# Optimization experiments

Hardware: AMD Instinct MI355X
Metric: run time of the kernel (lower is better)

The kernel has to match this reference:

```python
import jax, jax.numpy as jnp
import numpy as np


def setup_inputs() -> dict:
    key = jax.random.key(0)
    ks = jax.random.split(key, 8)
    T, B = 256, 256
    n_m, n_dT, nd, nx = 256, 256, 512, 512
    c = n_m + n_dT + nd  # 1024, RNNCell0 input/hidden size
    s = 0.05  # weight init scale
    return {
        "x": jax.random.normal(ks[0], (B, nx), jnp.float32),
        "M_flow": jax.random.normal(ks[1], (T, B, n_m), jnp.float32),
        "DT": jax.random.normal(ks[2], (T, B, n_dT), jnp.float32),
        "D": jax.random.normal(ks[3], (T, B, nd), jnp.float32),
        # cell0: RNNCell(c, c); cell1: RNNCell(c, nx); bias=False
        "W_ih0": jax.random.normal(ks[4], (c, c), jnp.float32) * s,
        "W_hh0": jax.random.normal(ks[5], (c, c), jnp.float32) * s,
        "W_ih1": jax.random.normal(ks[6], (nx, c), jnp.float32) * s,
        "W_hh1": jax.random.normal(ks[7], (nx, nx), jnp.float32) * s,
    }


def reference(x, M_flow, DT, D, W_ih0, W_hh0, W_ih1, W_hh1):
    # ins per step: cat([m_flow, dT, d], dim=1) -> (T, B, c)
    ins = jnp.concatenate([M_flow, DT, D], axis=2)
    # cell0 receives a freshly zeroed hidden state each step, so its
    # recurrent term W_hh0 @ 0 vanishes; the input->hidden GEMM is
    # therefore time-independent and can be batched over T.
    H = jax.nn.relu(jnp.einsum('tbc,dc->tbd', ins, W_ih0))  # (T, B, c)

    def step(x, h):
        # cell1: x' = relu(W_ih1 @ h + W_hh1 @ x)
        x = jax.nn.relu(h @ W_ih1.T + x @ W_hh1.T)
        return x, x

    _, X = jax.lax.scan(step, x, H)  # X: (T, B, nx)
    Y = X[:, :, -1]                  # y = x[:, -1] per step -> (T, B)
    return X, Y
```

## Files before the change

kernel.cpp:

```cpp
#include <hip/hip_runtime.h>

typedef __attribute__((ext_vector_type(8))) short short8;
typedef __attribute__((ext_vector_type(4))) float f32x4;
typedef __attribute__((ext_vector_type(4))) unsigned int u32x4;

__device__ __forceinline__ unsigned short f2bu(float x) {
  unsigned int u = __float_as_uint(x);
  u += 0x7fffu + ((u >> 16) & 1u);
  return (unsigned short)(u >> 16);
}
__device__ __forceinline__ unsigned int pk2(float a, float b) {
  return (unsigned int)f2bu(a) | ((unsigned int)f2bu(b) << 16);
}
__device__ __forceinline__ void gload_lds16(const void* g, void* l) {
  __builtin_amdgcn_global_load_lds((const __attribute__((address_space(1))) unsigned int*)g,
                                   (__attribute__((address_space(3))) unsigned int*)l, 16, 0, 0);
}
__device__ __forceinline__ void gload_lds16_coh(const void* g, void* l) {
  __builtin_amdgcn_global_load_lds((const __attribute__((address_space(1))) unsigned int*)g,
                                   (__attribute__((address_space(3))) unsigned int*)l, 16, 0, 17);
}
__device__ __forceinline__ void store16_coh(void* p, u32x4 v) {
  asm volatile("global_store_dwordx4 %0, %1, off sc0 sc1" :: "v"(p), "v"(v) : "memory");
}

__global__ void cast_concat_kernel(const float* __restrict__ Mf,
                                   const float* __restrict__ DTf,
                                   const float* __restrict__ Df,
                                   unsigned short* __restrict__ ins) {
  size_t idx = (size_t)blockIdx.x * blockDim.x + threadIdx.x;
  size_t e0 = idx * 8;
  size_t m = e0 >> 10;
  int c = (int)(e0 & 1023);
  const float* src;
  if (c < 256)      src = Mf  + m * 256 + c;
  else if (c < 512) src = DTf + m * 256 + (c - 256);
  else              src = Df  + m * 512 + (c - 512);
  float4 f0 = reinterpret_cast<const float4*>(src)[0];
  float4 f1 = reinterpret_cast<const float4*>(src)[1];
  uint4 o;
  o.x = pk2(f0.x, f0.y); o.y = pk2(f0.z, f0.w);
  o.z = pk2(f1.x, f1.y); o.w = pk2(f1.z, f1.w);
  *reinterpret_cast<uint4*>(ins + e0) = o;
}

__global__ void cast_w_kernel(const float* __restrict__ in, unsigned short* __restrict__ out, int n8) {
  int idx = blockIdx.x * blockDim.x + threadIdx.x;
  if (idx >= n8) return;
  const float* src = in + (size_t)idx * 8;
  float4 f0 = reinterpret_cast<const float4*>(src)[0];
  float4 f1 = reinterpret_cast<const float4*>(src)[1];
  uint4 o;
  o.x = pk2(f0.x, f0.y); o.y = pk2(f0.z, f0.w);
  o.z = pk2(f1.x, f1.y); o.w = pk2(f1.z, f1.w);
  *reinterpret_cast<uint4*>(out + (size_t)idx * 8) = o;
}

template <int RELU, typename TOUT>
__global__ __launch_bounds__(256) void gemm_bt_kernel(const unsigned short* __restrict__ A,
                                                      const unsigned short* __restrict__ Bt,
                                                      TOUT* __restrict__ C,
                                                      int M, int N, int K) {
  __shared__ unsigned short As[128 * 32];
  __shared__ unsigned short Bs[128 * 32];
  const int tid = threadIdx.x;
  const int l = tid & 63, w = tid >> 6;
  const int lr = l & 15, lg = l >> 4;
  const int wm = w >> 1, wn = w & 1;
  const int tiles_n = N >> 7;
  const int tm = blockIdx.x / tiles_n, tn = blockIdx.x % tiles_n;
  const int bm0 = tm << 7, bn0 = tn << 7;

  f32x4 acc[4][4] = {};

  for (int kt = 0; kt < K; kt += 32) {
#pragma unroll
    for (int i = 0; i < 2; ++i) {
      int ch = tid + (i << 8);
      int row = ch >> 2, cc = ch & 3;
      const unsigned short* ga = A + (size_t)(bm0 + row) * K + kt + cc * 8;
      const unsigned short* gb = Bt + (size_t)(bn0 + row) * K + kt + cc * 8;
      unsigned short* la = As + ((size_t)((i << 8) + (w << 6))) * 8;
      unsigned short* lb = Bs + ((size_t)((i << 8) + (w << 6))) * 8;
      gload_lds16(ga, la);
      gload_lds16(gb, lb);
    }
    __syncthreads();
    short8 af[4], bf[4];
#pragma unroll
    for (int mi = 0; mi < 4; ++mi)
      af[mi] = *reinterpret_cast<const short8*>(As + (wm * 64 + mi * 16 + lr) * 32 + lg * 8);
#pragma unroll
    for (int ni = 0; ni < 4; ++ni)
      bf[ni] = *reinterpret_cast<const short8*>(Bs + (wn * 64 + ni * 16 + lr) * 32 + lg * 8);
#pragma unroll
    for (int mi = 0; mi < 4; ++mi)
#pragma unroll
      for (int ni = 0; ni < 4; ++ni)
        acc[mi][ni] = __builtin_amdgcn_mfma_f32_16x16x32_bf16(af[mi], bf[ni], acc[mi][ni], 0, 0, 0);
    __syncthreads();
  }

#pragma unroll
  for (int mi = 0; mi < 4; ++mi)
#pragma unroll
    for (int ni = 0; ni < 4; ++ni)
#pragma unroll
      for (int r = 0; r < 4; ++r) {
        int row = bm0 + wm * 64 + mi * 16 + lg * 4 + r;
        int col = bn0 + wn * 64 + ni * 16 + lr;
        float v = acc[mi][ni][r];
        if (RELU) v = fmaxf(v, 0.f);
        if constexpr (sizeof(TOUT) == 2) {
          reinterpret_cast<unsigned short*>(C)[(size_t)row * N + col] = f2bu(v);
        } else {
          C[(size_t)row * N + col] = v;
        }
      }
}

__global__ void xscrub_kernel(char* xexb) {
  size_t idx = (size_t)blockIdx.x * blockDim.x + threadIdx.x;
  u32x4 z = {0, 0, 0, 0};
  store16_coh(xexb + idx * 16, z);
}

__global__ __launch_bounds__(256)
void recurrence_tf(const float* __restrict__ Whh1,
                   const float* __restrict__ x0f,
                   const float* __restrict__ G,
                   char* xexb,
                   float* __restrict__ X, float* __restrict__ Y) {
  __shared__ char smem[163840];
  const int tid = threadIdx.x;
  const int l = tid & 63, wv = tid >> 6;
  const int lr = l & 15, lg = l >> 4;
  const int bid = blockIdx.x;
  const int g = ((bid & 7) << 1) | ((bid >> 3) & 1);
  const int q = bid >> 4;
  const int r0 = g << 4;
  const int jbw = wv << 5;
  char* Wl = smem;
  char* xls0 = smem + 131072;
  char* xls1 = smem + 147456;

  {
    int j = tid >> 1;
    int kc0 = (tid & 1) << 8;
    const float* wr = Whh1 + (size_t)(128 * q + j) * 512 + kc0;
    int sw = (j & 7) << 4;
    for (int kk = 0; kk < 256; kk += 8) {
      float4 f0 = reinterpret_cast<const float4*>(wr + kk)[0];
      float4 f1 = reinterpret_cast<const float4*>(wr + kk)[1];
      uint4 o;
      o.x = pk2(f0.x, f0.y); o.y = pk2(f0.z, f0.w);
      o.z = pk2(f1.x, f1.y); o.w = pk2(f1.z, f1.w);
      *reinterpret_cast<uint4*>(Wl + j * 1024 + ((2 * (kc0 + kk)) ^ sw)) = o;
    }
  }
#pragma unroll
  for (int c = 0; c < 4; ++c) {
    int id = tid + (c << 8);
    int row = id >> 6;
    int kc = (id & 63) << 3;
    int qq = kc >> 7, kp = kc & 127;
    const float* src = x0f + (size_t)(r0 + row) * 512 + kc;
    float4 f0 = reinterpret_cast<const float4*>(src)[0];
    float4 f1 = reinterpret_cast<const float4*>(src)[1];
    uint4 o;
    o.x = pk2(f0.x, f0.y); o.y = pk2(f0.z, f0.w);
    o.z = pk2(f1.x, f1.y); o.w = pk2(f1.z, f1.w);
    *reinterpret_cast<uint4*>(xls0 + qq * 4096 + row * 256 +
                              ((2 * kp) ^ ((row & 7) << 4))) = o;
  }

  float gcur[8], gnxt[8];
#pragma unroll
  for (int jt = 0; jt < 2; ++jt)
#pragma unroll
    for (int r = 0; r < 4; ++r)
      gcur[jt * 4 + r] = G[((size_t)r0 + lg * 4 + r) * 512 + q * 128 + jbw + jt * 16 + lr];
  __syncthreads();

  const int swzR = (lr & 7) << 4;
  int rq[3];
  {
    int n = 0;
    for (int qq = 0; qq < 4; ++qq)
      if (qq != q) rq[n++] = qq;
  }
  float vsave[8];
  short8 arr[12];
  int ep = 1;

  for (int t = 0; t < 256; ++t) {
    char* xc = (t & 1) ? xls1 : xls0;
    const unsigned sh = (unsigned)(((t >> 1) & 1) << 16);
    const u32x4 e = {sh, sh ^ 0x10000u, sh, sh ^ 0x10000u};

    if (t) {
      float* Xp = X + ((size_t)(t - 1) * 256 + r0) * 512 + q * 128;
#pragma unroll
      for (int jt = 0; jt < 2; ++jt)
#pragma unroll
        for (int r = 0; r < 4; ++r)
          Xp[(size_t)(lg * 4 + r) * 512 + jbw + jt * 16 + lr] = vsave[jt * 4 + r];
      if (q == 3 && wv == 3 && lr == 15)
#pragma unroll
        for (int r = 0; r < 4; ++r)
          Y[(t - 1) * 256 + r0 + lg * 4 + r] = vsave[4 + r];
    }
    {
      int tn = (t < 255) ? t + 1 : t;
      const float* Gn = G + ((size_t)tn * 256 + r0) * 512 + q * 128;
#pragma unroll
      for (int jt = 0; jt < 2; ++jt)
#pragma unroll
        for (int r = 0; r < 4; ++r)
          gnxt[jt * 4 + r] = Gn[(size_t)(lg * 4 + r) * 512 + jbw + jt * 16 + lr];
    }

    f32x4 acc[2] = {};
    {
      short8 ao[4];
#pragma unroll
      for (int kp = 0; kp < 4; ++kp)
        ao[kp] = *reinterpret_cast<const short8*>(
            xc + q * 4096 + lr * 256 + ((kp * 64 + lg * 16) ^ swzR));
#pragma unroll
      for (int jt = 0; jt < 2; ++jt) {
        int jl = jbw + jt * 16 + lr;
        const char* wb = Wl + jl * 1024;
        int swj = (jl & 7) << 4;
#pragma unroll
        for (int kp = 0; kp < 4; ++kp) {
          short8 wf = *reinterpret_cast<const short8*>(
              wb + (((q * 4 + kp) * 64 + lg * 16) ^ swj));
          acc[jt] = __builtin_amdgcn_mfma_f32_16x16x32_bf16(ao[kp], wf, acc[jt], 0, 0, 0);
        }
      }
    }

    unsigned mybad = 0;
#define READCHECK()                                                           \
  {                                                                           \
    mybad = 0;                                                                \
    _Pragma("unroll") for (int m = 0; m < 3; ++m) {                           \
      int qq = rq[m];                                                         \
      _Pragma("unroll") for (int kp = 0; kp < 4; ++kp) {                      \
        short8 f = *reinterpret_cast<const short8*>(                          \
            xc + qq * 4096 + lr * 256 + ((kp * 64 + lg * 16) ^ swzR));        \
        arr[m * 4 + kp] = f;                                                  \
        u32x4 d = __builtin_bit_cast(u32x4, f);                               \
        u32x4 xr = (d ^ e) & 0x10000u;                                        \
        mybad |= xr.x | xr.y | xr.z | xr.w;                                   \
      }                                                                       \
    }                                                                         \
  }
    if (t) {
      const char* xsb = xexb + (((t & 1) * 16 + g) * 16384);
#pragma unroll
      for (int m = 0; m < 3; ++m)
        gload_lds16_coh(xsb + rq[m] * 4096 + wv * 1024 + (size_t)l * 16,
                        xc + rq[m] * 4096 + wv * 1024);
      asm volatile("s_waitcnt vmcnt(0)" ::: "memory");
      __builtin_amdgcn_sched_barrier(0);
      __syncthreads();
      READCHECK();
      int* badw = (int*)(xc + q * 4096);
      for (int it = 0; it < 64; ++it) {
        if (__any(mybad != 0)) { if (l == 0) *badw = ep; }
        __syncthreads();
        bool bad = (*badw == ep);
        ++ep;
        if (!bad) break;
#pragma unroll
        for (int m = 0; m < 3; ++m)
          gload_lds16_coh(xsb + rq[m] * 4096 + wv * 1024 + (size_t)l * 16,
                          xc + rq[m] * 4096 + wv * 1024);
        asm volatile("s_waitcnt vmcnt(0)" ::: "memory");
        __builtin_amdgcn_sched_barrier(0);
        __syncthreads();
        READCHECK();
      }
    } else {
      READCHECK();
    }
#undef READCHECK

#pragma unroll
    for (int m = 0; m < 3; ++m) {
      int qq = rq[m];
#pragma unroll
      for (int jt = 0; jt < 2; ++jt) {
        int jl = jbw + jt * 16 + lr;
        const char* wb = Wl + jl * 1024;
        int swj = (jl & 7) << 4;
#pragma unroll
        for (int kp = 0; kp < 4; ++kp) {
          short8 wf = *reinterpret_cast<const short8*>(
              wb + (((qq * 4 + kp) * 64 + lg * 16) ^ swj));
          acc[jt] = __builtin_amdgcn_mfma_f32_16x16x32_bf16(arr[m * 4 + kp], wf, acc[jt], 0, 0, 0);
        }
      }
    }

#pragma unroll
    for (int jt = 0; jt < 2; ++jt)
#pragma unroll
      for (int r = 0; r < 4; ++r)
        vsave[jt * 4 + r] = fmaxf(gcur[jt * 4 + r] + acc[jt][r], 0.f);
#pragma unroll
    for (int ee = 0; ee < 8; ++ee) gcur[ee] = gnxt[ee];

    if (t < 255) {
      char* xn = (t & 1) ? xls0 : xls1;
      const unsigned snext = (unsigned)(((t + 1) >> 1) & 1);
#pragma unroll
      for (int jt = 0; jt < 2; ++jt)
#pragma unroll
        for (int r = 0; r < 4; ++r) {
          float v = vsave[jt * 4 + r];
          float vn = __shfl_xor(v, 1);
          if (!(lr & 1)) {
            int i = lg * 4 + r;
            int jc = jbw + jt * 16 + lr;
            unsigned pv = pk2(v, vn);
            pv = (pv & ~0x10000u) | ((snext ^ (unsigned)((jc >> 1) & 1)) << 16);
            *reinterpret_cast<unsigned int*>(
                xn + q * 4096 + i * 256 + ((2 * jc) ^ ((i & 7) << 4))) = pv;
          }
        }
      __syncthreads();
      char* xd = xexb + ((((t + 1) & 1) * 16 + g) * 16384) + q * 4096;
      u32x4 val = *reinterpret_cast<const u32x4*>(xn + q * 4096 + tid * 16);
      store16_coh(xd + tid * 16, val);
    }
  }

  {
    float* Xp = X + ((size_t)255 * 256 + r0) * 512 + q * 128;
#pragma unroll
    for (int jt = 0; jt < 2; ++jt)
#pragma unroll
      for (int r = 0; r < 4; ++r)
        Xp[(size_t)(lg * 4 + r) * 512 + jbw + jt * 16 + lr] = vsave[jt * 4 + r];
    if (q == 3 && wv == 3 && lr == 15)
#pragma unroll
      for (int r = 0; r < 4; ++r)
        Y[255 * 256 + r0 + lg * 4 + r] = vsave[4 + r];
  }
}

extern "C" void kernel_launch(void* const* d_in, const int* in_sizes, int n_in,
                              void* d_out, int out_size, void* d_ws, size_t ws_size,
                              hipStream_t stream) {
  const float* x0   = (const float*)d_in[0];
  const float* Mf   = (const float*)d_in[1];
  const float* DTf  = (const float*)d_in[2];
  const float* Df   = (const float*)d_in[3];
  const float* Wih0 = (const float*)d_in[4];
  const float* Wih1 = (const float*)d_in[6];
  const float* Whh1 = (const float*)d_in[7];

  char* ws = (char*)d_ws;
  unsigned short* ins = (unsigned short*)(ws);
  unsigned short* H   = (unsigned short*)(ws + 134217728ULL);
  unsigned short* w0b = (unsigned short*)(ws + 268435456ULL);
  unsigned short* w1b = (unsigned short*)(ws + 270532608ULL);
  char* xex           = ws + 271581184ULL;
  float* G = (float*)(ws);

  xscrub_kernel<<<128, 256, 0, stream>>>(xex);
  cast_concat_kernel<<<32768, 256, 0, stream>>>(Mf, DTf, Df, ins);
  cast_w_kernel<<<512, 256, 0, stream>>>(Wih0, w0b, 131072);
  cast_w_kernel<<<256, 256, 0, stream>>>(Wih1, w1b, 65536);

  gemm_bt_kernel<1, unsigned short><<<(65536 / 128) * (1024 / 128), 256, 0, stream>>>(
      ins, w0b, H, 65536, 1024, 1024);
  gemm_bt_kernel<0, float><<<(65536 / 128) * (512 / 128), 256, 0, stream>>>(
      H, w1b, G, 65536, 512, 1024);

  float* X = (float*)d_out;
  float* Y = X + 33554432;
  recurrence_tf<<<64, 256, 0, stream>>>(Whh1, x0, G, xex, X, Y);
}
```

Measured before the change: 1.083 ms.

## Poll single flag word per stale partition and swizzle GEMM block order

The recurrent kernel's retry loop now tracks staleness per remote quarter. When a quarter is stale, it spins on a single coherent dword until the parity bit flips, then re-fetches only the stale quarters instead of reloading all three. This is meant to reduce redundant global reloads and barrier rounds while waiting for other blocks' results. Separately, the GEMM block index is remapped into groups of 8 M-tiles to improve L2 reuse. The spin poll assumes the first word's flag is representative, and that correctness depends on the write order of producers.

```diff
diff --git a/kernel.cpp b/kernel.cpp
--- a/kernel.cpp
+++ b/kernel.cpp
@@ -68,7 +68,9 @@
   const int lr = l & 15, lg = l >> 4;
   const int wm = w >> 1, wn = w & 1;
   const int tiles_n = N >> 7;
-  const int tm = blockIdx.x / tiles_n, tn = blockIdx.x % tiles_n;
+  const int S = tiles_n << 3;
+  const int sgrp = blockIdx.x / S, rr = blockIdx.x % S;
+  const int tm = (sgrp << 3) + (rr & 7), tn = rr >> 3;
   const int bm0 = tm << 7, bn0 = tn << 7;
 
   f32x4 acc[4][4] = {};
@@ -191,7 +193,7 @@
   }
   float vsave[8];
   short8 arr[12];
-  int ep = 1;
+  unsigned mb[3];
 
   for (int t = 0; t < 256; ++t) {
     char* xc = (t & 1) ? xls1 : xls0;
@@ -241,10 +243,9 @@
       }
     }
 
-    unsigned mybad = 0;
 #define READCHECK()                                                           \
   {                                                                           \
-    mybad = 0;                                                                \
+    mb[0] = mb[1] = mb[2] = 0;                                                \
     _Pragma("unroll") for (int m = 0; m < 3; ++m) {                           \
       int qq = rq[m];                                                         \
       _Pragma("unroll") for (int kp = 0; kp < 4; ++kp) {                      \
@@ -253,7 +254,7 @@
         arr[m * 4 + kp] = f;                                                  \
         u32x4 d = __builtin_bit_cast(u32x4, f);                               \
         u32x4 xr = (d ^ e) & 0x10000u;                                        \
-        mybad |= xr.x | xr.y | xr.z | xr.w;                                   \
+        mb[m] |= xr.x | xr.y | xr.z | xr.w;                                   \
       }                                                                       \
     }                                                                         \
   }
@@ -267,17 +268,30 @@
       __builtin_amdgcn_sched_barrier(0);
       __syncthreads();
       READCHECK();
-      int* badw = (int*)(xc + q * 4096);
+      volatile int* vw = (volatile int*)(xc + q * 4096);
       for (int it = 0; it < 64; ++it) {
-        if (__any(mybad != 0)) { if (l == 0) *badw = ep; }
+        unsigned wm = (__any(mb[0]) ? 1u : 0u) | (__any(mb[1]) ? 2u : 0u) |
+                      (__any(mb[2]) ? 4u : 0u);
+        if (l == 0) vw[wv] = (int)wm;
         __syncthreads();
-        bool bad = (*badw == ep);
-        ++ep;
-        if (!bad) break;
+        unsigned comb = (unsigned)(vw[0] | vw[1] | vw[2] | vw[3]) & 7u;
+        if (!comb) break;
 #pragma unroll
         for (int m = 0; m < 3; ++m)
-          gload_lds16_coh(xsb + rq[m] * 4096 + wv * 1024 + (size_t)l * 16,
-                          xc + rq[m] * 4096 + wv * 1024);
+          if (comb & (1u << m)) {
+            const unsigned* pp = (const unsigned*)(xsb + rq[m] * 4096);
+            unsigned pv;
+            do {
+              asm volatile("global_load_dword %0, %1, off sc0 sc1\n\t"
+                           "s_waitcnt vmcnt(0)"
+                           : "=&v"(pv) : "v"(pp) : "memory");
+            } while ((pv ^ sh) & 0x10000u);
+          }
+#pragma unroll
+        for (int m = 0; m < 3; ++m)
+          if (comb & (1u << m))
+            gload_lds16_coh(xsb + rq[m] * 4096 + wv * 1024 + (size_t)l * 16,
+                            xc + rq[m] * 4096 + wv * 1024);
         asm volatile("s_waitcnt vmcnt(0)" ::: "memory");
         __builtin_amdgcn_sched_barrier(0);
         __syncthreads();
```

Measured after the change: 1.101 ms. Within noise of the previous version (+1.7%).

## Replace 128x128 GEMM with 256x256 double-buffered, swizzled, interleaved-stage MFMA kernel

Applied to the files above, without the earlier changes.

Replaces the batched input-projection GEMM kernel with a 256x256-tile, 512-thread kernel. It uses a 64-wide K step, XOR-swizzled LDS layout, and two-stage prefetch via global_load_lds. The next tiles are staged in chunks between MFMA groups, with setprio and manual waitcnt/barriers, so global loads overlap compute. Block indices are grouped so consecutive blocks share A rows for L2 reuse. The aim is higher arithmetic intensity and less exposed load latency, at the cost of heavier register and LDS use and fragile hand-tuned synchronization.

```diff
diff --git a/kernel.cpp b/kernel.cpp
--- a/kernel.cpp
+++ b/kernel.cpp
@@ -57,57 +57,156 @@
 }
 
 template <int RELU, typename TOUT>
-__global__ __launch_bounds__(256) void gemm_bt_kernel(const unsigned short* __restrict__ A,
-                                                      const unsigned short* __restrict__ Bt,
-                                                      TOUT* __restrict__ C,
-                                                      int M, int N, int K) {
-  __shared__ unsigned short As[128 * 32];
-  __shared__ unsigned short Bs[128 * 32];
+__global__ __launch_bounds__(512, 2) void gemm256_kernel(
+    const unsigned short* __restrict__ A, const unsigned short* __restrict__ Bt,
+    TOUT* __restrict__ C, int M, int N, int K) {
+  __shared__ unsigned short lds[2][2][16384];
   const int tid = threadIdx.x;
   const int l = tid & 63, w = tid >> 6;
   const int lr = l & 15, lg = l >> 4;
-  const int wm = w >> 1, wn = w & 1;
-  const int tiles_n = N >> 7;
-  const int tm = blockIdx.x / tiles_n, tn = blockIdx.x % tiles_n;
-  const int bm0 = tm << 7, bn0 = tn << 7;
-
-  f32x4 acc[4][4] = {};
-
-  for (int kt = 0; kt < K; kt += 32) {
-#pragma unroll
-    for (int i = 0; i < 2; ++i) {
-      int ch = tid + (i << 8);
-      int row = ch >> 2, cc = ch & 3;
-      const unsigned short* ga = A + (size_t)(bm0 + row) * K + kt + cc * 8;
-      const unsigned short* gb = Bt + (size_t)(bn0 + row) * K + kt + cc * 8;
-      unsigned short* la = As + ((size_t)((i << 8) + (w << 6))) * 8;
-      unsigned short* lb = Bs + ((size_t)((i << 8) + (w << 6))) * 8;
-      gload_lds16(ga, la);
-      gload_lds16(gb, lb);
-    }
-    __syncthreads();
-    short8 af[4], bf[4];
-#pragma unroll
-    for (int mi = 0; mi < 4; ++mi)
-      af[mi] = *reinterpret_cast<const short8*>(As + (wm * 64 + mi * 16 + lr) * 32 + lg * 8);
+  const int wm = w >> 2, wn = w & 3;
+  const int tiles_n = N >> 8;
+  const int S = tiles_n << 3;
+  const int sgrp = blockIdx.x / S, rr = blockIdx.x % S;
+  const int tm = (sgrp << 3) + (rr & 7), tn = rr >> 3;
+  const int bm0 = tm << 8, bn0 = tn << 8;
+  const int NT = K >> 6;
+  const unsigned short* Ab = A + (size_t)bm0 * K;
+  const unsigned short* Bb = Bt + (size_t)bn0 * K;
+  const int srow = l >> 3;
+  const int scol = ((l & 7) ^ srow) << 3;
+  const int swz = lr & 7;
+
+  f32x4 acc[8][4] = {};
+
+#define STG8(SRC, R0, LDSS, KT2)                                              \
+  gload_lds16((SRC) + (size_t)((R0) + srow) * K + ((KT2) << 6) + scol,        \
+              (LDSS) + (R0) * 64)
+
+#pragma unroll
+  for (int t0 = 0; t0 < 2; ++t0) {
+    unsigned short* As_ = lds[t0][0];
+    unsigned short* Bs_ = lds[t0][1];
+    STG8(Ab, (w << 3), As_, t0);
+    STG8(Ab, 128 + (w << 3), As_, t0);
+    STG8(Ab, 64 + (w << 3), As_, t0);
+    STG8(Ab, 192 + (w << 3), As_, t0);
+    STG8(Bb, (w << 3), Bs_, t0);
+    STG8(Bb, 64 + (w << 3), Bs_, t0);
+    STG8(Bb, 128 + (w << 3), Bs_, t0);
+    STG8(Bb, 192 + (w << 3), Bs_, t0);
+  }
+  asm volatile("s_waitcnt vmcnt(8)" ::: "memory");
+  __builtin_amdgcn_s_barrier();
+
+  for (int kt = 0; kt < NT; ++kt) {
+    const unsigned short* Asd = lds[kt & 1][0];
+    const unsigned short* Bsd = lds[kt & 1][1];
+    unsigned short* Asn = lds[kt & 1][0];
+    unsigned short* Bsn = lds[kt & 1][1];
+    const int kt2 = kt + 2;
+    const bool dostg = kt2 < NT;
+
+    short8 a[4][2], b[4][2];
+#pragma unroll
+    for (int i = 0; i < 4; ++i) {
+      int row = wm * 128 + i * 16 + lr;
+#pragma unroll
+      for (int s = 0; s < 2; ++s)
+        a[i][s] = *reinterpret_cast<const short8*>(
+            Asd + row * 64 + ((((s << 2) + lg) ^ swz) << 3));
+    }
+#pragma unroll
+    for (int ni = 0; ni < 4; ++ni) {
+      int row = wn * 64 + ni * 16 + lr;
+#pragma unroll
+      for (int s = 0; s < 2; ++s)
+        b[ni][s] = *reinterpret_cast<const short8*>(
+            Bsd + row * 64 + ((((s << 2) + lg) ^ swz) << 3));
+    }
+    asm volatile("s_waitcnt lgkmcnt(0)" ::: "memory");
+    __builtin_amdgcn_sched_barrier(0);
+    __builtin_amdgcn_s_setprio(1);
+#pragma unroll
+    for (int ni = 0; ni < 2; ++ni)
+#pragma unroll
+      for (int i = 0; i < 4; ++i)
+#pragma unroll
+        for (int s = 0; s < 2; ++s)
+          acc[i][ni] = __builtin_amdgcn_mfma_f32_16x16x32_bf16(a[i][s], b[ni][s], acc[i][ni], 0, 0, 0);
+    __builtin_amdgcn_s_setprio(0);
+    __builtin_amdgcn_s_barrier();
+
+    if (dostg) {
+      STG8(Ab, (w << 3), Asn, kt2);
+      STG8(Ab, 128 + (w << 3), Asn, kt2);
+      STG8(Bb, (w << 3), Bsn, kt2);
+      STG8(Bb, 64 + (w << 3), Bsn, kt2);
+    }
+    __builtin_amdgcn_s_setprio(1);
+#pragma unroll
+    for (int ni = 2; ni < 4; ++ni)
+#pragma unroll
+      for (int i = 0; i < 4; ++i)
+#pragma unroll
+        for (int s = 0; s < 2; ++s)
+          acc[i][ni] = __builtin_amdgcn_mfma_f32_16x16x32_bf16(a[i][s], b[ni][s], acc[i][ni], 0, 0, 0);
+    __builtin_amdgcn_s_setprio(0);
+    __builtin_amdgcn_s_barrier();
+
+#pragma unroll
+    for (int i = 0; i < 4; ++i) {
+      int row = wm * 128 + 64 + i * 16 + lr;
+#pragma unroll
+      for (int s = 0; s < 2; ++s)
+        a[i][s] = *reinterpret_cast<const short8*>(
+            Asd + row * 64 + ((((s << 2) + lg) ^ swz) << 3));
+    }
+    if (dostg) {
+      STG8(Bb, 128 + (w << 3), Bsn, kt2);
+      STG8(Bb, 192 + (w << 3), Bsn, kt2);
+    }
+    asm volatile("s_waitcnt lgkmcnt(0)" ::: "memory");
+    __builtin_amdgcn_sched_barrier(0);
+    __builtin_amdgcn_s_setprio(1);
+#pragma unroll
+    for (int ni = 0; ni < 2; ++ni)
+#pragma unroll
+      for (int i = 0; i < 4; ++i)
+#pragma unroll
+        for (int s = 0; s < 2; ++s)
+          acc[4 + i][ni] = __builtin_amdgcn_mfma_f32_16x16x32_bf16(a[i][s], b[ni][s], acc[4 + i][ni], 0, 0, 0);
+    __builtin_amdgcn_s_setprio(0);
+    __builtin_amdgcn_s_barrier();
+
+    if (dostg) {
+      STG8(Ab, 64 + (w << 3), Asn, kt2);
+      STG8(Ab, 192 + (w << 3), Asn, kt2);
+    }
+    __builtin_amdgcn_s_setprio(1);
+#pragma unroll
+    for (int ni = 2; ni < 4; ++ni)
+#pragma unroll
+      for (int i = 0; i < 4; ++i)
+#pragma unroll
+        for (int s = 0; s < 2; ++s)
+          acc[4 + i][ni] = __builtin_amdgcn_mfma_f32_16x16x32_bf16(a[i][s], b[ni][s], acc[4 + i][ni], 0, 0, 0);
+    __builtin_amdgcn_s_setprio(0);
+    if (kt + 2 < NT)
+      asm volatile("s_waitcnt vmcnt(8)" ::: "memory");
+    else
+      asm volatile("s_waitcnt vmcnt(0)" ::: "memory");
+    __builtin_amdgcn_s_barrier();
+  }
+#undef STG8
+
+#pragma unroll
+  for (int mi = 0; mi < 8; ++mi)
 #pragma unroll
     for (int ni = 0; ni < 4; ++ni)
-      bf[ni] = *reinterpret_cast<const short8*>(Bs + (wn * 64 + ni * 16 + lr) * 32 + lg * 8);
-#pragma unroll
-    for (int mi = 0; mi < 4; ++mi)
-#pragma unroll
-      for (int ni = 0; ni < 4; ++ni)
-        acc[mi][ni] = __builtin_amdgcn_mfma_f32_16x16x32_bf16(af[mi], bf[ni], acc[mi][ni], 0, 0, 0);
-    __syncthreads();
-  }
-
-#pragma unroll
-  for (int mi = 0; mi < 4; ++mi)
-#pragma unroll
-    for (int ni = 0; ni < 4; ++ni)
 #pragma unroll
       for (int r = 0; r < 4; ++r) {
-        int row = bm0 + wm * 64 + mi * 16 + lg * 4 + r;
+        int row = bm0 + wm * 128 + mi * 16 + lg * 4 + r;
         int col = bn0 + wn * 64 + ni * 16 + lr;
         float v = acc[mi][ni][r];
         if (RELU) v = fmaxf(v, 0.f);
@@ -376,9 +475,9 @@
   cast_w_kernel<<<512, 256, 0, stream>>>(Wih0, w0b, 131072);
   cast_w_kernel<<<256, 256, 0, stream>>>(Wih1, w1b, 65536);
 
-  gemm_bt_kernel<1, unsigned short><<<(65536 / 128) * (1024 / 128), 256, 0, stream>>>(
+  gemm256_kernel<1, unsigned short><<<(65536 / 256) * (1024 / 256), 512, 0, stream>>>(
       ins, w0b, H, 65536, 1024, 1024);
-  gemm_bt_kernel<0, float><<<(65536 / 128) * (512 / 128), 256, 0, stream>>>(
+  gemm256_kernel<0, float><<<(65536 / 256) * (512 / 256), 512, 0, stream>>>(
       H, w1b, G, 65536, 512, 1024);
 
   float* X = (float*)d_out;
```

After: 959.8 us. 1.13x faster.
